# Performance work log

Measured on AMD Instinct MI355X. Metric: run time of the kernel, lower is better.

Reference implementation:

```python
import jax, jax.numpy as jnp
import numpy as np

H = 256  # hidden_dim


def _mlp(x, w1, b1, w2, b2):
    # Linear -> ReLU -> (Dropout=identity in eval) -> Linear
    return jax.nn.relu(x @ w1 + b1) @ w2 + b2


def setup_inputs() -> dict:
    key = jax.random.key(0)
    ks = jax.random.split(key, 9)
    bsz, seq = 32, 4096
    s = 1.0 / np.sqrt(2 * H)
    inp = {
        "h": jax.random.normal(ks[0], (bsz, seq, H), dtype=jnp.float32),
        "mask": jnp.ones((bsz, seq), dtype=jnp.float32),
        "ew1": jax.random.uniform(ks[1], (2 * H, H), minval=-s, maxval=s),
        "eb1": jax.random.uniform(ks[2], (H,), minval=-s, maxval=s),
        "ew2": jax.random.uniform(ks[3], (H, H), minval=-s, maxval=s),
        "eb2": jax.random.uniform(ks[4], (H,), minval=-s, maxval=s),
        "nw1": jax.random.uniform(ks[5], (2 * H, H), minval=-s, maxval=s),
        "nb1": jax.random.uniform(ks[6], (H,), minval=-s, maxval=s),
        "nw2": jax.random.uniform(ks[7], (H, H), minval=-s, maxval=s),
        "nb2": jax.random.uniform(ks[8], (H,), minval=-s, maxval=s),
    }
    return inp


def reference(h, mask, ew1, eb1, ew2, eb2, nw1, nb1, nw2, nb2):
    left = h[:, :-1, :]   # [B, S-1, H]
    right = h[:, 1:, :]   # [B, S-1, H]
    m_lr = _mlp(jnp.concatenate([left, right], axis=-1), ew1, eb1, ew2, eb2)
    m_rl = _mlp(jnp.concatenate([right, left], axis=-1), ew1, eb1, ew2, eb2)
    # shifted scatter-add: agg[:,1:] += m_lr ; agg[:,:-1] += m_rl
    zcol = jnp.zeros_like(h[:, :1, :])
    agg = jnp.concatenate([zcol, m_lr], axis=1) + jnp.concatenate([m_rl, zcol], axis=1)
    updated = _mlp(jnp.concatenate([h, agg], axis=-1), nw1, nb1, nw2, nb2)
    updated = updated * mask[:, :, None]
    return h + updated
```

## Files before the change

kernel.cpp:

```cpp
#include <hip/hip_runtime.h>
#include <hip/hip_bf16.h>

typedef __bf16 bf16_t;
typedef bf16_t bf16x8 __attribute__((ext_vector_type(8)));
typedef bf16_t bf16x4 __attribute__((ext_vector_type(4)));
typedef float f32x4 __attribute__((ext_vector_type(4)));

#define SEQ 4096
#define BSZ 32
#define T_TOK 64
#define PROWS 66
#define LSTR 264

#define OFF_X 0
#define OFF_A (66 * LSTR)
#define OFF_B (132 * LSTR)
#define OFF_S (198 * LSTR)
#define SMEM_ELEMS (262 * LSTR)
#define SMEM_BYTES (SMEM_ELEMS * 2)

#define W1F 0
#define NAF 131072
#define WBF 196608
#define N2F 262144
#define B2N 327680

#define BAR() asm volatile("s_waitcnt lgkmcnt(0)\n\ts_barrier" ::: "memory")

__global__ void wprep(const float* __restrict__ ew1, const float* __restrict__ nw1,
                      const float* __restrict__ nw2, bf16_t* __restrict__ wsw) {
    int idx = blockIdx.x * 256 + threadIdx.x;
    int region, rel, outbase;
    if (idx < 131072)      { region = 0; rel = idx;          outbase = W1F; }
    else if (idx < 196608) { region = 1; rel = idx - 131072; outbase = NAF; }
    else                   { region = 2; rel = idx - 196608; outbase = N2F; }
    int f = rel >> 9, o = rel & 511;
    int l = o >> 3, e = o & 7;
    int r = l & 15, kg = l >> 4;
    int nt = f >> 3, ks = f & 7;
    int k = ks * 32 + kg * 8 + e;
    int n = nt * 16 + r;
    float v;
    if (region == 0)
        v = (nt < 16) ? ew1[k * 256 + n] : ew1[(256 + k) * 256 + (n - 256)];
    else if (region == 1)
        v = nw1[k * 256 + n];
    else
        v = nw2[k * 256 + n];
    wsw[outbase + rel] = (bf16_t)v;
}

__global__ void wprep2(const float* __restrict__ ew2, const float* __restrict__ eb2,
                       const float* __restrict__ nw1, bf16_t* __restrict__ wsw) {
    int k = blockIdx.x;
    int n = threadIdx.x;
    if (k < 256) {
        float acc = 0.f;
        for (int j = 0; j < 256; ++j)
            acc += ew2[k * 256 + j] * nw1[(256 + j) * 256 + n];
        int ks = k >> 5, kg = (k >> 3) & 3, e = k & 7;
        int nt = n >> 4, r = n & 15;
        wsw[WBF + ((nt * 8 + ks) << 9) + ((kg * 16 + r) << 3) + e] = (bf16_t)acc;
    } else {
        float acc = 0.f;
        for (int j = 0; j < 256; ++j)
            acc += eb2[j] * nw1[(256 + j) * 256 + n];
        ((float*)(wsw + B2N))[n] = acc;
    }
}

__launch_bounds__(512, 2)
__global__ void gnl_kernel(const float* __restrict__ h, const float* __restrict__ mask,
                           const float* __restrict__ eb1, const float* __restrict__ nb1,
                           const float* __restrict__ nb2,
                           const bf16_t* __restrict__ wsw, float* __restrict__ out) {
    extern __shared__ bf16_t sm[];

    const int tid   = threadIdx.x;
    const int lane  = tid & 63;
    const int w     = tid >> 6;
    const int batch = blockIdx.x >> 6;
    const int tile  = blockIdx.x & 63;
    const int t0    = tile * T_TOK;
    const long baseTok = (long)batch * SEQ;

    const int c   = lane & 15;
    const int kg  = lane >> 4;
    const int crb = kg << 2;
    const int n0a = w * 16;
    const int n0b = (w + 8) * 16;

    auto loadw = [&](bf16x8 (&f)[8], int base, int nt) {
#pragma unroll
        for (int ks = 0; ks < 8; ++ks)
            f[ks] = *(const bf16x8*)(wsw + base + ((nt * 8 + ks) << 9) + (lane << 3));
    };
    auto loada = [&](bf16x8 (&f)[8], int poff, int rbase) {
        const bf16_t* p = sm + poff + (rbase + c) * LSTR + (kg << 3);
#pragma unroll
        for (int ks = 0; ks < 8; ++ks) f[ks] = *(const bf16x8*)(p + (ks << 5));
    };
    auto mfma2 = [&](bf16x8 (&f)[8], bf16x8 (&wa)[8], bf16x8 (&wb)[8],
                     f32x4& a0, f32x4& a1) {
        __builtin_amdgcn_s_setprio(1);
#pragma unroll
        for (int ks = 0; ks < 8; ++ks) {
            a0 = __builtin_amdgcn_mfma_f32_16x16x32_bf16(wa[ks], f[ks], a0, 0, 0, 0);
            a1 = __builtin_amdgcn_mfma_f32_16x16x32_bf16(wb[ks], f[ks], a1, 0, 0, 0);
        }
        __builtin_amdgcn_s_setprio(0);
    };

    bf16x8 wa0[8], wb0[8];
    loadw(wa0, W1F, w);
    loadw(wb0, W1F, w + 8);

    for (int cc = tid; cc < PROWS * 32; cc += 512) {
        int r = cc >> 5;
        int fc = (cc & 31) << 3;
        int t = t0 - 1 + r;
        bf16x8 v;
        if (t >= 0 && t < SEQ) {
            const float* src = h + (((long)(baseTok + t)) << 8) + fc;
            float4 x0 = ((const float4*)src)[0];
            float4 x1 = ((const float4*)src)[1];
            v[0] = (bf16_t)x0.x; v[1] = (bf16_t)x0.y;
            v[2] = (bf16_t)x0.z; v[3] = (bf16_t)x0.w;
            v[4] = (bf16_t)x1.x; v[5] = (bf16_t)x1.y;
            v[6] = (bf16_t)x1.z; v[7] = (bf16_t)x1.w;
        } else {
#pragma unroll
            for (int q = 0; q < 8; ++q) v[q] = (bf16_t)0.0f;
        }
        *(bf16x8*)(sm + OFF_X + r * LSTR + fc) = v;
    }
    BAR();

#pragma unroll
    for (int p = 0; p < 2; ++p) {
        bf16x8 wa[8], wb[8];
        if (p == 0) {
#pragma unroll
            for (int ks = 0; ks < 8; ++ks) { wa[ks] = wa0[ks]; wb[ks] = wb0[ks]; }
        } else {
            loadw(wa, W1F, w + 16);
            loadw(wb, W1F, w + 24);
        }
        int poff = p ? OFF_B : OFF_A;
        bf16x8 fA[8], fB[8];
        loada(fA, OFF_X, 0);
#pragma unroll
        for (int mt = 0; mt < 5; ++mt) {
            bf16x8 (&cur)[8] = (mt & 1) ? fB : fA;
            bf16x8 (&nxt)[8] = (mt & 1) ? fA : fB;
            if (mt < 4) loada(nxt, OFF_X, (mt + 1) * 16);
            f32x4 aA = {0.f, 0.f, 0.f, 0.f}, aB = {0.f, 0.f, 0.f, 0.f};
            mfma2(cur, wa, wb, aA, aB);
            int row = mt * 16 + c;
            if (row < PROWS) {
                bf16x4 pA, pB;
#pragma unroll
                for (int q = 0; q < 4; ++q) { pA[q] = (bf16_t)aA[q]; pB[q] = (bf16_t)aB[q]; }
                *(bf16x4*)(sm + poff + row * LSTR + n0a + crb) = pA;
                *(bf16x4*)(sm + poff + row * LSTR + n0b + crb) = pB;
            }
        }
    }

    f32x4 ha[4][2];
    {
        bf16x8 na[8], nb8[8];
        loadw(na, NAF, w);
        loadw(nb8, NAF, w + 8);
        bf16x8 fA[8], fB[8];
        loada(fA, OFF_X, 1);
#pragma unroll
        for (int tm = 0; tm < 4; ++tm) {
            bf16x8 (&cur)[8] = (tm & 1) ? fB : fA;
            bf16x8 (&nxt)[8] = (tm & 1) ? fA : fB;
            if (tm < 3) loada(nxt, OFF_X, tm * 16 + 17);
            f32x4 a0 = {0.f, 0.f, 0.f, 0.f}, a1 = {0.f, 0.f, 0.f, 0.f};
            mfma2(cur, na, nb8, a0, a1);
            ha[tm][0] = a0; ha[tm][1] = a1;
        }
    }

    bf16x8 wba[8], wbb[8];
    loadw(wba, WBF, w);
    loadw(wbb, WBF, w + 8);
    BAR();

#pragma unroll
    for (int it = 0; it < 4; ++it) {
        int cc = tid + it * 512;
        int i = cc >> 5;
        int fc = (cc & 31) << 3;
        float bl = (t0 + i >= 1) ? 1.f : 0.f;
        float br = (t0 + i <= SEQ - 2) ? 1.f : 0.f;
        bf16x8 aL = *(const bf16x8*)(sm + OFF_A + i * LSTR + fc);
        bf16x8 aR = *(const bf16x8*)(sm + OFF_A + (i + 2) * LSTR + fc);
        bf16x8 bC = *(const bf16x8*)(sm + OFF_B + (i + 1) * LSTR + fc);
        float4 b1a = *(const float4*)(eb1 + fc);
        float4 b1b = *(const float4*)(eb1 + fc + 4);
        bf16x8 sv;
#pragma unroll
        for (int q = 0; q < 8; ++q) {
            float b1f = (q < 4) ? ((const float*)&b1a)[q] : ((const float*)&b1b)[q - 4];
            float x = (float)bC[q] + b1f;
            float l = fmaxf((float)aL[q] + x, 0.f) * bl;
            float r = fmaxf((float)aR[q] + x, 0.f) * br;
            sv[q] = (bf16_t)(l + r);
        }
        *(bf16x8*)(sm + OFF_S + i * LSTR + fc) = sv;
    }
    BAR();

    {
        float4 n1a = *(const float4*)(nb1 + n0a + crb);
        float4 n1b = *(const float4*)(nb1 + n0b + crb);
        const float* b2n = (const float*)(wsw + B2N);
        float4 c2a = *(const float4*)(b2n + n0a + crb);
        float4 c2b = *(const float4*)(b2n + n0b + crb);
        bf16x8 fA[8], fB[8];
        loada(fA, OFF_S, 0);
#pragma unroll
        for (int tm = 0; tm < 4; ++tm) {
            bf16x8 (&cur)[8] = (tm & 1) ? fB : fA;
            bf16x8 (&nxt)[8] = (tm & 1) ? fA : fB;
            if (tm < 3) loada(nxt, OFF_S, (tm + 1) * 16);
            f32x4 a0 = ha[tm][0], a1 = ha[tm][1];
            mfma2(cur, wba, wbb, a0, a1);
            int row = tm * 16 + c;
            int t = t0 + row;
            float cnt = ((t >= 1) ? 1.f : 0.f) + ((t <= SEQ - 2) ? 1.f : 0.f);
            bf16x4 p0, p1;
#pragma unroll
            for (int q = 0; q < 4; ++q) {
                p0[q] = (bf16_t)fmaxf(a0[q] + ((const float*)&n1a)[q] + cnt * ((const float*)&c2a)[q], 0.f);
                p1[q] = (bf16_t)fmaxf(a1[q] + ((const float*)&n1b)[q] + cnt * ((const float*)&c2b)[q], 0.f);
            }
            *(bf16x4*)(sm + OFF_A + row * LSTR + n0a + crb) = p0;
            *(bf16x4*)(sm + OFF_A + row * LSTR + n0b + crb) = p1;
        }
    }
    bf16x8 n2a[8], n2b[8];
    loadw(n2a, N2F, w);
    loadw(n2b, N2F, w + 8);
    BAR();

    {
        float4 v2a = *(const float4*)(nb2 + n0a + crb);
        float4 v2b = *(const float4*)(nb2 + n0b + crb);
        bf16x8 fA[8], fB[8];
        loada(fA, OFF_A, 0);
#pragma unroll
        for (int tm = 0; tm < 4; ++tm) {
            long t = baseTok + t0 + tm * 16 + c;
            float m = mask[t];
            bf16x8 (&cur)[8] = (tm & 1) ? fB : fA;
            bf16x8 (&nxt)[8] = (tm & 1) ? fA : fB;
            if (tm < 3) loada(nxt, OFF_A, (tm + 1) * 16);
            f32x4 a0 = {0.f, 0.f, 0.f, 0.f}, a1 = {0.f, 0.f, 0.f, 0.f};
            mfma2(cur, n2a, n2b, a0, a1);
            int rrow = tm * 16 + c + 1;
            bf16x4 r0 = *(const bf16x4*)(sm + OFF_X + rrow * LSTR + n0a + crb);
            bf16x4 r1 = *(const bf16x4*)(sm + OFF_X + rrow * LSTR + n0b + crb);
            long g0 = (t << 8) + n0a + crb;
            long g1 = (t << 8) + n0b + crb;
            float4 o0, o1;
            o0.x = (float)r0[0] + m * (a0[0] + v2a.x);
            o0.y = (float)r0[1] + m * (a0[1] + v2a.y);
            o0.z = (float)r0[2] + m * (a0[2] + v2a.z);
            o0.w = (float)r0[3] + m * (a0[3] + v2a.w);
            o1.x = (float)r1[0] + m * (a1[0] + v2b.x);
            o1.y = (float)r1[1] + m * (a1[1] + v2b.y);
            o1.z = (float)r1[2] + m * (a1[2] + v2b.z);
            o1.w = (float)r1[3] + m * (a1[3] + v2b.w);
            *(float4*)(out + g0) = o0;
            *(float4*)(out + g1) = o1;
        }
    }
}

extern "C" void kernel_launch(void* const* d_in, const int* in_sizes, int n_in,
                              void* d_out, int out_size, void* d_ws, size_t ws_size,
                              hipStream_t stream) {
    const float* h    = (const float*)d_in[0];
    const float* mask = (const float*)d_in[1];
    const float* ew1  = (const float*)d_in[2];
    const float* eb1  = (const float*)d_in[3];
    const float* ew2  = (const float*)d_in[4];
    const float* eb2  = (const float*)d_in[5];
    const float* nw1  = (const float*)d_in[6];
    const float* nb1  = (const float*)d_in[7];
    const float* nw2  = (const float*)d_in[8];
    const float* nb2  = (const float*)d_in[9];
    float* out   = (float*)d_out;
    bf16_t* wsw  = (bf16_t*)d_ws;

    wprep<<<1024, 256, 0, stream>>>(ew1, nw1, nw2, wsw);
    wprep2<<<257, 256, 0, stream>>>(ew2, eb2, nw1, wsw);

    hipFuncSetAttribute(reinterpret_cast<const void*>(gnl_kernel),
                        hipFuncAttributeMaxDynamicSharedMemorySize, SMEM_BYTES);

    gnl_kernel<<<BSZ * (SEQ / T_TOK), 512, SMEM_BYTES, stream>>>(
        h, mask, eb1, nb1, nb2, wsw, out);
}
```

Baseline: 163.6 us.

## Shrink token tile to 48 and reuse LDS panel to cut shared memory

```diff
diff --git a/kernel.cpp b/kernel.cpp
--- a/kernel.cpp
+++ b/kernel.cpp
@@ -8,15 +8,16 @@
 
 #define SEQ 4096
 #define BSZ 32
-#define T_TOK 64
-#define PROWS 66
+#define T_TOK 48
+#define TILES 86
+#define PROWS 50
 #define LSTR 264
+#define NPANEL (PROWS * LSTR)
 
 #define OFF_X 0
-#define OFF_A (66 * LSTR)
-#define OFF_B (132 * LSTR)
-#define OFF_S (198 * LSTR)
-#define SMEM_ELEMS (262 * LSTR)
+#define OFF_A NPANEL
+#define OFF_B (2 * NPANEL)
+#define SMEM_ELEMS (3 * NPANEL)
 #define SMEM_BYTES (SMEM_ELEMS * 2)
 
 #define W1F 0
@@ -79,8 +80,8 @@
     const int tid   = threadIdx.x;
     const int lane  = tid & 63;
     const int w     = tid >> 6;
-    const int batch = blockIdx.x >> 6;
-    const int tile  = blockIdx.x & 63;
+    const int batch = blockIdx.x / TILES;
+    const int tile  = blockIdx.x % TILES;
     const int t0    = tile * T_TOK;
     const long baseTok = (long)batch * SEQ;
 
@@ -115,24 +116,28 @@
     loadw(wa0, W1F, w);
     loadw(wb0, W1F, w + 8);
 
-    for (int cc = tid; cc < PROWS * 32; cc += 512) {
-        int r = cc >> 5;
-        int fc = (cc & 31) << 3;
-        int t = t0 - 1 + r;
-        bf16x8 v;
-        if (t >= 0 && t < SEQ) {
-            const float* src = h + (((long)(baseTok + t)) << 8) + fc;
-            float4 x0 = ((const float4*)src)[0];
-            float4 x1 = ((const float4*)src)[1];
-            v[0] = (bf16_t)x0.x; v[1] = (bf16_t)x0.y;
-            v[2] = (bf16_t)x0.z; v[3] = (bf16_t)x0.w;
-            v[4] = (bf16_t)x1.x; v[5] = (bf16_t)x1.y;
-            v[6] = (bf16_t)x1.z; v[7] = (bf16_t)x1.w;
-        } else {
-#pragma unroll
-            for (int q = 0; q < 8; ++q) v[q] = (bf16_t)0.0f;
-        }
-        *(bf16x8*)(sm + OFF_X + r * LSTR + fc) = v;
+#pragma unroll
+    for (int it = 0; it < 4; ++it) {
+        int cc = tid + it * 512;
+        if (cc < PROWS * 32) {
+            int r = cc >> 5;
+            int fc = (cc & 31) << 3;
+            int t = t0 - 1 + r;
+            bf16x8 v;
+            if (t >= 0 && t < SEQ) {
+                const float* src = h + (((long)(baseTok + t)) << 8) + fc;
+                float4 x0 = ((const float4*)src)[0];
+                float4 x1 = ((const float4*)src)[1];
+                v[0] = (bf16_t)x0.x; v[1] = (bf16_t)x0.y;
+                v[2] = (bf16_t)x0.z; v[3] = (bf16_t)x0.w;
+                v[4] = (bf16_t)x1.x; v[5] = (bf16_t)x1.y;
+                v[6] = (bf16_t)x1.z; v[7] = (bf16_t)x1.w;
+            } else {
+#pragma unroll
+                for (int q = 0; q < 8; ++q) v[q] = (bf16_t)0.0f;
+            }
+            *(bf16x8*)(sm + OFF_X + r * LSTR + fc) = v;
+        }
     }
     BAR();
 
@@ -150,10 +155,10 @@
         bf16x8 fA[8], fB[8];
         loada(fA, OFF_X, 0);
 #pragma unroll
-        for (int mt = 0; mt < 5; ++mt) {
+        for (int mt = 0; mt < 4; ++mt) {
             bf16x8 (&cur)[8] = (mt & 1) ? fB : fA;
             bf16x8 (&nxt)[8] = (mt & 1) ? fA : fB;
-            if (mt < 4) loada(nxt, OFF_X, (mt + 1) * 16);
+            if (mt < 3) loada(nxt, OFF_X, (mt + 1) * 16);
             f32x4 aA = {0.f, 0.f, 0.f, 0.f}, aB = {0.f, 0.f, 0.f, 0.f};
             mfma2(cur, wa, wb, aA, aB);
             int row = mt * 16 + c;
@@ -167,7 +172,7 @@
         }
     }
 
-    f32x4 ha[4][2];
+    f32x4 ha[3][2];
     {
         bf16x8 na[8], nb8[8];
         loadw(na, NAF, w);
@@ -175,10 +180,10 @@
         bf16x8 fA[8], fB[8];
         loada(fA, OFF_X, 1);
 #pragma unroll
-        for (int tm = 0; tm < 4; ++tm) {
+        for (int tm = 0; tm < 3; ++tm) {
             bf16x8 (&cur)[8] = (tm & 1) ? fB : fA;
             bf16x8 (&nxt)[8] = (tm & 1) ? fA : fB;
-            if (tm < 3) loada(nxt, OFF_X, tm * 16 + 17);
+            if (tm < 2) loada(nxt, OFF_X, tm * 16 + 17);
             f32x4 a0 = {0.f, 0.f, 0.f, 0.f}, a1 = {0.f, 0.f, 0.f, 0.f};
             mfma2(cur, na, nb8, a0, a1);
             ha[tm][0] = a0; ha[tm][1] = a1;
@@ -190,8 +195,9 @@
     loadw(wbb, WBF, w + 8);
     BAR();
 
-#pragma unroll
-    for (int it = 0; it < 4; ++it) {
+    bf16x8 svr[3];
+#pragma unroll
+    for (int it = 0; it < 3; ++it) {
         int cc = tid + it * 512;
         int i = cc >> 5;
         int fc = (cc & 31) << 3;
@@ -211,7 +217,15 @@
             float r = fmaxf((float)aR[q] + x, 0.f) * br;
             sv[q] = (bf16_t)(l + r);
         }
-        *(bf16x8*)(sm + OFF_S + i * LSTR + fc) = sv;
+        svr[it] = sv;
+    }
+    BAR();
+#pragma unroll
+    for (int it = 0; it < 3; ++it) {
+        int cc = tid + it * 512;
+        int i = cc >> 5;
+        int fc = (cc & 31) << 3;
+        *(bf16x8*)(sm + OFF_B + i * LSTR + fc) = svr[it];
     }
     BAR();
 
@@ -222,12 +236,12 @@
         float4 c2a = *(const float4*)(b2n + n0a + crb);
         float4 c2b = *(const float4*)(b2n + n0b + crb);
         bf16x8 fA[8], fB[8];
-        loada(fA, OFF_S, 0);
-#pragma unroll
-        for (int tm = 0; tm < 4; ++tm) {
+        loada(fA, OFF_B, 0);
+#pragma unroll
+        for (int tm = 0; tm < 3; ++tm) {
             bf16x8 (&cur)[8] = (tm & 1) ? fB : fA;
             bf16x8 (&nxt)[8] = (tm & 1) ? fA : fB;
-            if (tm < 3) loada(nxt, OFF_S, (tm + 1) * 16);
+            if (tm < 2) loada(nxt, OFF_B, (tm + 1) * 16);
             f32x4 a0 = ha[tm][0], a1 = ha[tm][1];
             mfma2(cur, wba, wbb, a0, a1);
             int row = tm * 16 + c;
@@ -254,30 +268,35 @@
         bf16x8 fA[8], fB[8];
         loada(fA, OFF_A, 0);
 #pragma unroll
-        for (int tm = 0; tm < 4; ++tm) {
-            long t = baseTok + t0 + tm * 16 + c;
+        for (int tm = 0; tm < 3; ++tm) {
+            int row = tm * 16 + c;
+            int tok = t0 + row;
+            int tokc = (tok < SEQ) ? tok : (SEQ - 1);
+            long t = baseTok + tokc;
             float m = mask[t];
             bf16x8 (&cur)[8] = (tm & 1) ? fB : fA;
             bf16x8 (&nxt)[8] = (tm & 1) ? fA : fB;
-            if (tm < 3) loada(nxt, OFF_A, (tm + 1) * 16);
+            if (tm < 2) loada(nxt, OFF_A, (tm + 1) * 16);
             f32x4 a0 = {0.f, 0.f, 0.f, 0.f}, a1 = {0.f, 0.f, 0.f, 0.f};
             mfma2(cur, n2a, n2b, a0, a1);
-            int rrow = tm * 16 + c + 1;
+            int rrow = row + 1;
             bf16x4 r0 = *(const bf16x4*)(sm + OFF_X + rrow * LSTR + n0a + crb);
             bf16x4 r1 = *(const bf16x4*)(sm + OFF_X + rrow * LSTR + n0b + crb);
-            long g0 = (t << 8) + n0a + crb;
-            long g1 = (t << 8) + n0b + crb;
-            float4 o0, o1;
-            o0.x = (float)r0[0] + m * (a0[0] + v2a.x);
-            o0.y = (float)r0[1] + m * (a0[1] + v2a.y);
-            o0.z = (float)r0[2] + m * (a0[2] + v2a.z);
-            o0.w = (float)r0[3] + m * (a0[3] + v2a.w);
-            o1.x = (float)r1[0] + m * (a1[0] + v2b.x);
-            o1.y = (float)r1[1] + m * (a1[1] + v2b.y);
-            o1.z = (float)r1[2] + m * (a1[2] + v2b.z);
-            o1.w = (float)r1[3] + m * (a1[3] + v2b.w);
-            *(float4*)(out + g0) = o0;
-            *(float4*)(out + g1) = o1;
+            if (tok < SEQ) {
+                long g0 = (t << 8) + n0a + crb;
+                long g1 = (t << 8) + n0b + crb;
+                float4 o0, o1;
+                o0.x = (float)r0[0] + m * (a0[0] + v2a.x);
+                o0.y = (float)r0[1] + m * (a0[1] + v2a.y);
+                o0.z = (float)r0[2] + m * (a0[2] + v2a.z);
+                o0.w = (float)r0[3] + m * (a0[3] + v2a.w);
+                o1.x = (float)r1[0] + m * (a1[0] + v2b.x);
+                o1.y = (float)r1[1] + m * (a1[1] + v2b.y);
+                o1.z = (float)r1[2] + m * (a1[2] + v2b.z);
+                o1.w = (float)r1[3] + m * (a1[3] + v2b.w);
+                *(float4*)(out + g0) = o0;
+                *(float4*)(out + g1) = o1;
+            }
         }
     }
 }
@@ -304,6 +323,6 @@
     hipFuncSetAttribute(reinterpret_cast<const void*>(gnl_kernel),
                         hipFuncAttributeMaxDynamicSharedMemorySize, SMEM_BYTES);
 
-    gnl_kernel<<<BSZ * (SEQ / T_TOK), 512, SMEM_BYTES, stream>>>(
+    gnl_kernel<<<BSZ * TILES, 512, SMEM_BYTES, stream>>>(
         h, mask, eb1, nb1, nb2, wsw, out);
 }
```

Measured after the change: 159.6 us. 2.4% less time.
